# Kernel tuning notes

Measured on AMD Instinct MI355X. Metric: run time of the kernel, lower is better.

The kernel has to match this reference:

```python
import jax, jax.numpy as jnp
import numpy as np

DIM = 64
NB = 32
LEFT, RIGHT = -1.0, 1.0
EPS_BIN = 0.01
EPS_SLOPE = 0.01


def setup_inputs() -> dict:
    key = jax.random.key(0)
    ks = jax.random.split(key, 10)
    m, cdim, hid = 16384, 64, 100
    x = jax.random.uniform(ks[0], (m, DIM), minval=LEFT + 1e-3, maxval=RIGHT - 1e-3)
    cond = jax.random.normal(ks[1], (m, cdim))
    def dense(k, i, o, scale=1.0):
        return (jax.random.normal(k, (i, o)) * (scale / np.sqrt(i))).astype(jnp.float32)
    inp = dict(
        x=x, cond=cond,
        periodic_mask=jnp.ones((1, DIM), dtype=jnp.int32),
        w_W1=dense(ks[2], cdim, hid), w_b1=jnp.zeros((hid,), jnp.float32),
        w_W2=dense(ks[3], hid, DIM * NB, 0.1), w_b2=jnp.zeros((DIM * NB,), jnp.float32),
        h_W1=dense(ks[4], cdim, hid), h_b1=jnp.zeros((hid,), jnp.float32),
        h_W2=dense(ks[5], hid, DIM * NB, 0.1), h_b2=jnp.zeros((DIM * NB,), jnp.float32),
        s_W1=dense(ks[6], cdim, hid), s_b1=jnp.zeros((hid,), jnp.float32),
        s_W2=dense(ks[7], hid, DIM * (NB + 1), 0.1), s_b2=jnp.zeros((DIM * (NB + 1),), jnp.float32),
    )
    return inp


def _mlp(c, W1, b1, W2, b2):
    return jax.nn.silu(c @ W1 + b1) @ W2 + b2


def _rq_spline(x, w_logit, h_logit, d_raw, periodic_mask):
    # x: [m, dim]; w/h: [m, dim, NB]; d: [m, dim, NB+1]
    widths = EPS_BIN + (1.0 - EPS_BIN * NB) * jax.nn.softmax(w_logit, axis=-1)
    heights = EPS_BIN + (1.0 - EPS_BIN * NB) * jax.nn.softmax(h_logit, axis=-1)
    derivs = EPS_SLOPE + jax.nn.softplus(d_raw)  # [m, dim, NB+1]
    # periodic dims: tie boundary slopes (last == first)
    pm = periodic_mask.astype(bool)  # [1, dim]
    derivs = derivs.at[..., -1].set(jnp.where(pm, derivs[..., 0], derivs[..., -1]))

    span = RIGHT - LEFT
    cw = LEFT + span * jnp.concatenate(
        [jnp.zeros_like(widths[..., :1]), jnp.cumsum(widths, axis=-1)], axis=-1)
    ch = LEFT + span * jnp.concatenate(
        [jnp.zeros_like(heights[..., :1]), jnp.cumsum(heights, axis=-1)], axis=-1)
    cw = cw.at[..., 0].set(LEFT).at[..., -1].set(RIGHT)
    ch = ch.at[..., 0].set(LEFT).at[..., -1].set(RIGHT)
    wk_all = cw[..., 1:] - cw[..., :-1]   # actual bin widths
    hk_all = ch[..., 1:] - ch[..., :-1]   # actual bin heights

    # bin search: number of interior knots <= x
    idx = jnp.sum((x[..., None] >= cw[..., 1:-1]).astype(jnp.int32), axis=-1)
    idx = jnp.clip(idx, 0, NB - 1)[..., None]  # [m, dim, 1]

    gather = lambda a: jnp.take_along_axis(a, idx, axis=-1)[..., 0]
    cwk = gather(cw[..., :-1])
    chk = gather(ch[..., :-1])
    wk = gather(wk_all)
    hk = gather(hk_all)
    dk = gather(derivs[..., :-1])
    dk1 = gather(derivs[..., 1:])

    delta = hk / wk
    theta = (x - cwk) / wk
    t1m = theta * (1.0 - theta)
    denom = delta + (dk1 + dk - 2.0 * delta) * t1m
    y = chk + hk * (delta * theta * theta + dk * t1m) / denom
    deriv = (delta * delta) * (dk1 * theta * theta + 2.0 * delta * t1m
                               + dk * (1.0 - theta) * (1.0 - theta)) / (denom * denom)
    ladJ = jnp.sum(jnp.log(deriv), axis=-1, keepdims=True)  # [m, 1]
    return y, ladJ


def reference(x, cond, periodic_mask, w_W1, w_b1, w_W2, w_b2,
              h_W1, h_b1, h_W2, h_b2, s_W1, s_b1, s_W2, s_b2):
    m = x.shape[0]
    w = _mlp(cond, w_W1, w_b1, w_W2, w_b2).reshape(m, DIM, NB)
    h = _mlp(cond, h_W1, h_b1, h_W2, h_b2).reshape(m, DIM, NB)
    s = _mlp(cond, s_W1, s_b1, s_W2, s_b2).reshape(m, DIM, NB + 1)
    return _rq_spline(x, w, h, s, periodic_mask)
```

## Files before the change

### kernel.cpp

```cpp
#include <hip/hip_runtime.h>
#include <stdint.h>

#define M_TOTAL 16384
#define DIMS    64
#define CDIM    64
#define HID     100
#define ROWS    32
#define LOG2E   1.4426950408889634f
#define LN2     0.6931471805599453f

typedef __bf16 bf16x8 __attribute__((ext_vector_type(8)));
typedef float  f32x4  __attribute__((ext_vector_type(4)));

#define BKG        14
#define CN_STRIDE  (BKG*16*8)
#define DIM_STRIDE (7*CN_STRIDE)
#define W2M_ELEMS  (DIMS*DIM_STRIDE)
#define B2ALL_ELEMS (DIMS*128)
#define W1M_ELEMS  (3*7*8*16*8)
#define B1_ELEMS   (3*112)
#define W2M_OFF   0
#define B2ALL_OFF (W2M_ELEMS*2)
#define W1M_OFF   (B2ALL_OFF + B2ALL_ELEMS*4)
#define B1_OFF    (W1M_OFF + W1M_ELEMS*2)

__device__ __forceinline__ uint16_t f2bf(float f) {
  uint32_t u = __float_as_uint(f);
  return (uint16_t)((u + 0x8000u) >> 16);
}

__global__ void repack_kernel(
    const float* __restrict__ wW2, const float* __restrict__ wb2,
    const float* __restrict__ hW2, const float* __restrict__ hb2,
    const float* __restrict__ sW2, const float* __restrict__ sb2,
    const float* __restrict__ wW1, const float* __restrict__ hW1,
    const float* __restrict__ sW1,
    const float* __restrict__ wb1, const float* __restrict__ hb1,
    const float* __restrict__ sb1,
    uint16_t* __restrict__ W2m, float* __restrict__ b2all,
    uint16_t* __restrict__ W1m, float* __restrict__ b1all)
{
  int i = blockIdx.x * 256 + threadIdx.x;
  if (i < W2M_ELEMS) {
    int j  = i & 7;
    int c  = (i >> 3) & 15;
    int t  = i >> 7;
    int kg = t % BKG;
    int t2 = t / BKG;
    int cn = t2 % 7;
    int d  = t2 / 7;
    int k   = kg*8 + j;
    int col = cn*16 + c;
    float v = 0.f;
    if (k < HID) {
      if (col < 32)      v = wW2[k*2048 + d*32 + col] * LOG2E;
      else if (col < 64) v = hW2[k*2048 + d*32 + (col-32)] * LOG2E;
      else if (col < 97) v = sW2[k*2112 + d*33 + (col-64)];
    }
    W2m[i] = f2bf(v);
    return;
  }
  i -= W2M_ELEMS;
  if (i < B2ALL_ELEMS) {
    int c = i & 127;
    int d = i >> 7;
    float v = 0.f;
    if (c < 32)      v = wb2[d*32 + c] * LOG2E;
    else if (c < 64) v = hb2[d*32 + (c-32)] * LOG2E;
    else if (c < 97) v = sb2[d*33 + (c-64)];
    b2all[i] = v;
    return;
  }
  i -= B2ALL_ELEMS;
  if (i < W1M_ELEMS) {
    int jj = i & 7;
    int c  = (i >> 3) & 15;
    int kg = (i >> 7) & 7;
    int t  = i >> 10;
    int cn = t % 7;
    int mat = t / 7;
    int j = cn*16 + c;
    int k = kg*8 + jj;
    const float* W1 = (mat == 0) ? wW1 : (mat == 1) ? hW1 : sW1;
    W1m[i] = f2bf((j < HID) ? W1[k*HID + j] : 0.f);
    return;
  }
  i -= W1M_ELEMS;
  if (i < B1_ELEMS) {
    int mat = i / 112, col = i % 112;
    const float* b1 = (mat == 0) ? wb1 : (mat == 1) ? hb1 : sb1;
    b1all[i] = (col < HID) ? b1[col] : 0.f;
  }
}

__global__ __launch_bounds__(256, 2)
void spline_main(
    const float* __restrict__ X, const float* __restrict__ C,
    const int* __restrict__ pmask,
    const uint16_t* __restrict__ W2m, const float* __restrict__ b2all,
    const uint16_t* __restrict__ W1m, const float* __restrict__ b1all,
    float* __restrict__ Y, float* __restrict__ LADJ)
{
  __shared__ union {
    float cond_s[ROWS*68];
    float Ls[4][ROWS*100];
  } U;
  __shared__ uint16_t At[3*16*ROWS*8];
  __shared__ float LjLds[4][ROWS];

  const int tid = threadIdx.x;
  const int r0 = blockIdx.x * ROWS;
  const int lane = tid & 63, wv = tid >> 6;
  const int l15 = lane & 15, lkg = lane >> 4;
  const int hb = lane >> 5;
  const int srow = lane & 31;

  for (int i = tid; i < ROWS*CDIM; i += 256) {
    int r = i >> 6, c = i & 63;
    U.cond_s[r*68 + c] = C[(size_t)(r0 + r)*CDIM + c];
  }
  __syncthreads();

  {
    bf16x8 cf[2][2];
#pragma unroll
    for (int m = 0; m < 2; ++m)
#pragma unroll
      for (int ks = 0; ks < 2; ++ks) {
        const float* cp = &U.cond_s[(m*16 + l15)*68 + ks*32 + lkg*8];
        float4 c0 = *(const float4*)cp;
        float4 c1 = *(const float4*)(cp + 4);
        union { uint16_t u[8]; bf16x8 v; } tmp;
        tmp.u[0]=f2bf(c0.x); tmp.u[1]=f2bf(c0.y); tmp.u[2]=f2bf(c0.z); tmp.u[3]=f2bf(c0.w);
        tmp.u[4]=f2bf(c1.x); tmp.u[5]=f2bf(c1.y); tmp.u[6]=f2bf(c1.z); tmp.u[7]=f2bf(c1.w);
        cf[m][ks] = tmp.v;
      }
    for (int t = wv; t < 21; t += 4) {
      int mat = t / 7, cn = t % 7;
      const uint16_t* Wb = W1m + (size_t)(mat*7 + cn)*1024;
      bf16x8 wf[2];
#pragma unroll
      for (int ks = 0; ks < 2; ++ks)
        wf[ks] = *(const bf16x8*)&Wb[(ks*4 + lkg)*128 + l15*8];
      f32x4 h0 = {0.f,0.f,0.f,0.f}, h1 = {0.f,0.f,0.f,0.f};
#pragma unroll
      for (int ks = 0; ks < 2; ++ks) {
        h0 = __builtin_amdgcn_mfma_f32_16x16x32_bf16(cf[0][ks], wf[ks], h0, 0, 0, 0);
        h1 = __builtin_amdgcn_mfma_f32_16x16x32_bf16(cf[1][ks], wf[ks], h1, 0, 0, 0);
      }
      float bb = b1all[mat*112 + cn*16 + l15];
      int j = cn*16 + l15;
      int base = mat*4096 + (j >> 3)*256 + (j & 7);
#pragma unroll
      for (int r = 0; r < 4; ++r) {
        float a0 = h0[r] + bb;
        float v0 = a0 * __builtin_amdgcn_rcpf(1.f + __builtin_amdgcn_exp2f(-LOG2E*a0));
        At[base + (lkg*4 + r)*8] = f2bf(v0);
        float a1 = h1[r] + bb;
        float v1 = a1 * __builtin_amdgcn_rcpf(1.f + __builtin_amdgcn_exp2f(-LOG2E*a1));
        At[base + (16 + lkg*4 + r)*8] = f2bf(v1);
      }
    }
    for (int i2 = tid; i2 < 768; i2 += 256) {
      int mat = i2 >> 8, q = i2 & 255;
      *(uint32_t*)&At[mat*4096 + 14*256 + q*2] = 0u;
    }
  }
  __syncthreads();

  float* LsW = &U.Ls[wv][0];
  const int dbase = wv*16;
  float ladj2 = 0.f;
  float xq = 0.f; int pq = 0;

  auto SPLINE = [&](int d, float xv, int pm) {
    const float* Lr = LsW + srow*100 + hb*32;
    float e[32];
#pragma unroll
    for (int q = 0; q < 8; ++q) *(float4*)&e[4*q] = *(const float4*)(Lr + 4*q);
    float t2[16], t4[8], t8[4], t16[2];
#pragma unroll
    for (int k = 0; k < 16; ++k) t2[k] = e[2*k] + e[2*k+1];
#pragma unroll
    for (int k = 0; k < 8; ++k)  t4[k] = t2[2*k] + t2[2*k+1];
#pragma unroll
    for (int k = 0; k < 4; ++k)  t8[k] = t4[2*k] + t4[2*k+1];
    t16[0] = t8[0] + t8[1]; t16[1] = t8[2] + t8[3];
    float S = t16[0] + t16[1];
    float rs = __builtin_amdgcn_rcpf(S);
    float Aa = (xv + 1.f) * 0.7352941176470588f * S;
    float Uq = 0.014705882352941176f * S;

    float T = Aa, p = 0.f, fidx;
    {
      float A = fmaf(-16.f, Uq, T);
      bool c4 = t16[0] <= A;
      p = c4 ? t16[0] : p;  T = c4 ? A : T;

      float n8 = c4 ? t8[2] : t8[0];
      A = fmaf(-8.f, Uq, T);
      float tt = p + n8;
      bool c3 = tt <= A;
      p = c3 ? tt : p;  T = c3 ? A : T;

      float n4 = c4 ? (c3 ? t4[6] : t4[4]) : (c3 ? t4[2] : t4[0]);
      A = fmaf(-4.f, Uq, T);
      tt = p + n4;
      bool c2 = tt <= A;
      p = c2 ? tt : p;  T = c2 ? A : T;

      float n2 = c4 ? (c3 ? (c2 ? t2[14] : t2[12]) : (c2 ? t2[10] : t2[8]))
                    : (c3 ? (c2 ? t2[6]  : t2[4])  : (c2 ? t2[2]  : t2[0]));
      A = fmaf(-2.f, Uq, T);
      tt = p + n2;
      bool c1 = tt <= A;
      p = c1 ? tt : p;  T = c1 ? A : T;

      float n1 = c4 ? (c3 ? (c2 ? (c1 ? e[30] : e[28]) : (c1 ? e[26] : e[24]))
                          : (c2 ? (c1 ? e[22] : e[20]) : (c1 ? e[18] : e[16])))
                    : (c3 ? (c2 ? (c1 ? e[14] : e[12]) : (c1 ? e[10] : e[8]))
                          : (c2 ? (c1 ? e[6]  : e[4])  : (c1 ? e[2]  : e[0])));
      A = fmaf(-1.f, Uq, T);
      bool c0 = (p + n1) <= A;
      fidx = (c4 ? 16.f : 0.f) + (c3 ? 8.f : 0.f) + (c2 ? 4.f : 0.f)
           + (c1 ? 2.f : 0.f) + (c0 ? 1.f : 0.f);
    }
    float idxu = __shfl(fidx, srow);
    bool B4 = idxu >= 15.5f; float u = B4 ? idxu - 16.f : idxu;
    bool B3 = u >= 7.5f;  u = B3 ? u - 8.f : u;
    bool B2 = u >= 3.5f;  u = B2 ? u - 4.f : u;
    bool B1 = u >= 1.5f;  u = B1 ? u - 2.f : u;
    bool B0 = u >= 0.5f;
    float Psel = B4 ? t16[0] : 0.f;
    float q8 = B4 ? t8[2] : t8[0];
    Psel = B3 ? Psel + q8 : Psel;
    float q4 = B4 ? (B3 ? t4[6] : t4[4]) : (B3 ? t4[2] : t4[0]);
    Psel = B2 ? Psel + q4 : Psel;
    float q2 = B4 ? (B3 ? (B2 ? t2[14] : t2[12]) : (B2 ? t2[10] : t2[8]))
                  : (B3 ? (B2 ? t2[6]  : t2[4])  : (B2 ? t2[2]  : t2[0]));
    Psel = B1 ? Psel + q2 : Psel;
    float q1e = B4 ? (B3 ? (B2 ? (B1 ? e[28] : e[24]) : (B1 ? e[20] : e[16]))
                         : (B2 ? (B1 ? e[12] : e[8])  : (B1 ? e[4]  : e[0])))
                   : (B3 ? (B2 ? (B1 ? e[28-16] : e[24-16]) : (B1 ? e[4] : e[0])) : 0.f);
    q1e = B4 ? (B3 ? (B2 ? (B1 ? e[30-2] : e[26-2]) : (B1 ? e[22-2] : e[18-2]))
                   : (B2 ? (B1 ? e[14+16-2] : e[10+16-2]) : (B1 ? e[6+16-2] : e[2+16-2])))
             : (B3 ? (B2 ? (B1 ? e[14] : e[12]) : (B1 ? e[10] : e[8]))
                   : (B2 ? (B1 ? e[6] : e[4]) : (B1 ? e[2] : e[0])));
    {
      float a0_ = B1 ? e[2]  : e[0];
      float a1_ = B1 ? e[6]  : e[4];
      float a2_ = B1 ? e[10] : e[8];
      float a3_ = B1 ? e[14] : e[12];
      float a4_ = B1 ? e[18] : e[16];
      float a5_ = B1 ? e[22] : e[20];
      float a6_ = B1 ? e[26] : e[24];
      float a7_ = B1 ? e[30] : e[28];
      float b0_ = B2 ? a1_ : a0_;
      float b1_ = B2 ? a3_ : a2_;
      float b2_ = B2 ? a5_ : a4_;
      float b3_ = B2 ? a7_ : a6_;
      float c0_ = B3 ? b1_ : b0_;
      float c1_ = B3 ? b3_ : b2_;
      q1e = B4 ? c1_ : c0_;
    }
    float q1o;
    {
      float a0_ = B1 ? e[3]  : e[1];
      float a1_ = B1 ? e[7]  : e[5];
      float a2_ = B1 ? e[11] : e[9];
      float a3_ = B1 ? e[15] : e[13];
      float a4_ = B1 ? e[19] : e[17];
      float a5_ = B1 ? e[23] : e[21];
      float a6_ = B1 ? e[27] : e[25];
      float a7_ = B1 ? e[31] : e[29];
      float b0_ = B2 ? a1_ : a0_;
      float b1_ = B2 ? a3_ : a2_;
      float b2_ = B2 ? a5_ : a4_;
      float b3_ = B2 ? a7_ : a6_;
      float c0_ = B3 ? b1_ : b0_;
      float c1_ = B3 ? b3_ : b2_;
      q1o = B4 ? c1_ : c0_;
    }
    Psel = B0 ? Psel + q1e : Psel;
    float esel = B0 ? q1o : q1e;

    float cK = fmaf(0.02f, idxu, -1.f) + 1.36f*rs*Psel;
    float wK = (idxu > 30.5f) ? (1.f - cK) : fmaf(1.36f*rs, esel, 0.02f);
    int idxi = (int)idxu;
    int off = 64 + idxi + hb;
    if (hb && idxi == 31) off = pm ? 64 : 96;
    float sl = LsW[srow*100 + off];
    float dkv = fmaf(LN2, __builtin_amdgcn_logf(1.f + __builtin_amdgcn_exp2f(LOG2E*sl)), 0.01f);
    float cO = __shfl_xor(cK, 32);
    float wO = __shfl_xor(wK, 32);
    float dO = __shfl_xor(dkv, 32);
    float cwk = cK, wk = wK, dk = dkv, chk = cO, hk = wO, dk1 = dO;
    float rw = __builtin_amdgcn_rcpf(wk);
    float th = (xv - cwk)*rw;
    float delta = hk*rw;
    float omt = 1.f - th, t1m = th*omt, th2 = th*th;
    float denom = fmaf(dk1 + dk - 2.f*delta, t1m, delta);
    float rden = __builtin_amdgcn_rcpf(denom);
    float yv = fmaf(hk*fmaf(delta, th2, dk*t1m), rden, chk);
    float dn2 = fmaf(dk1, th2, fmaf(2.f*delta, t1m, dk*omt*omt));
    ladj2 += 2.f*(__builtin_amdgcn_logf(delta) - __builtin_amdgcn_logf(denom))
           + __builtin_amdgcn_logf(dn2);
    if (!hb) Y[(size_t)(r0 + srow)*DIMS + d] = yv;
  };

  auto LOADA = [&](bf16x8 (&a2)[2][4], int mat) {
#pragma unroll
    for (int m = 0; m < 2; ++m)
#pragma unroll
      for (int ks = 0; ks < 4; ++ks)
        a2[m][ks] = *(const bf16x8*)&At[mat*4096 + (ks*4 + lkg)*256 + (m*16 + l15)*8];
  };

  auto DO = [&](const bf16x8 (&afm)[2][4], const bf16x8 (&B)[4],
                float bb, int col, bool doexp) {
    f32x4 a0 = {bb,bb,bb,bb}, a1 = {bb,bb,bb,bb};
#pragma unroll
    for (int ks = 0; ks < 4; ++ks)
      a0 = __builtin_amdgcn_mfma_f32_16x16x32_bf16(afm[0][ks], B[ks], a0, 0, 0, 0);
#pragma unroll
    for (int ks = 0; ks < 4; ++ks)
      a1 = __builtin_amdgcn_mfma_f32_16x16x32_bf16(afm[1][ks], B[ks], a1, 0, 0, 0);
    if (doexp) {
#pragma unroll
      for (int r = 0; r < 4; ++r) {
        a0[r] = __builtin_amdgcn_exp2f(a0[r]);
        a1[r] = __builtin_amdgcn_exp2f(a1[r]);
      }
    }
    if (col < 97) {
#pragma unroll
      for (int r = 0; r < 4; ++r) {
        LsW[(lkg*4 + r)*100 + col]      = a0[r];
        LsW[(16 + lkg*4 + r)*100 + col] = a1[r];
      }
    }
  };

#pragma unroll 1
  for (int dd = 0; dd < 16; ++dd) {
    const int d = dbase + dd;
    const uint16_t* Bd = W2m + (size_t)d*DIM_STRIDE;
    auto LOADB = [&](bf16x8 (&dst)[4], int cn) {
#pragma unroll
      for (int ks = 0; ks < 4; ++ks) {
        int kgb = ks*4 + lkg; kgb = (kgb > 13) ? 13 : kgb;
        dst[ks] = *(const bf16x8*)&Bd[cn*CN_STRIDE + kgb*128 + l15*8];
      }
    };
    bf16x8 bA[4], bB[4], bC[4];
    LOADB(bA, 0); LOADB(bB, 1); LOADB(bC, 2);
    float bbv[7];
#pragma unroll
    for (int cn = 0; cn < 7; ++cn) bbv[cn] = b2all[d*128 + cn*16 + l15];
    float xn = X[(size_t)(r0 + srow)*DIMS + d];
    int pn = pmask[d];

    if (dd > 0) SPLINE(d - 1, xq, pq);
    xq = xn; pq = pn;

    bf16x8 afc[2][4];
    LOADA(afc, 0);
    DO(afc, bA, bbv[0], 0*16 + l15, true);  LOADB(bA, 3);
    DO(afc, bB, bbv[1], 1*16 + l15, true);  LOADB(bB, 4);
    LOADA(afc, 1);
    DO(afc, bC, bbv[2], 2*16 + l15, true);  LOADB(bC, 5);
    DO(afc, bA, bbv[3], 3*16 + l15, true);  LOADB(bA, 6);
    LOADA(afc, 2);
    DO(afc, bB, bbv[4], 4*16 + l15, false);
    DO(afc, bC, bbv[5], 5*16 + l15, false);
    DO(afc, bA, bbv[6], 6*16 + l15, false);
  }
  SPLINE(dbase + 15, xq, pq);

  if (!hb) LjLds[wv][srow] = ladj2;
  __syncthreads();
  if (tid < ROWS)
    LADJ[r0 + tid] = LN2 * ((LjLds[0][tid] + LjLds[1][tid]) + (LjLds[2][tid] + LjLds[3][tid]));
}

extern "C" void kernel_launch(void* const* d_in, const int* in_sizes, int n_in,
                              void* d_out, int out_size, void* d_ws, size_t ws_size,
                              hipStream_t stream) {
  const float* x     = (const float*)d_in[0];
  const float* cond  = (const float*)d_in[1];
  const int*   pmask = (const int*)d_in[2];
  const float* wW1 = (const float*)d_in[3];
  const float* wb1 = (const float*)d_in[4];
  const float* wW2 = (const float*)d_in[5];
  const float* wb2 = (const float*)d_in[6];
  const float* hW1 = (const float*)d_in[7];
  const float* hb1 = (const float*)d_in[8];
  const float* hW2 = (const float*)d_in[9];
  const float* hb2 = (const float*)d_in[10];
  const float* sW1 = (const float*)d_in[11];
  const float* sb1 = (const float*)d_in[12];
  const float* sW2 = (const float*)d_in[13];
  const float* sb2 = (const float*)d_in[14];

  uint16_t* W2m   = (uint16_t*)((char*)d_ws + W2M_OFF);
  float*    b2all = (float*)((char*)d_ws + B2ALL_OFF);
  uint16_t* W1m   = (uint16_t*)((char*)d_ws + W1M_OFF);
  float*    b1all = (float*)((char*)d_ws + B1_OFF);

  const int total = W2M_ELEMS + B2ALL_ELEMS + W1M_ELEMS + B1_ELEMS;
  repack_kernel<<<(total + 255)/256, 256, 0, stream>>>(
      wW2, wb2, hW2, hb2, sW2, sb2, wW1, hW1, sW1, wb1, hb1, sb1,
      W2m, b2all, W1m, b1all);

  float* Y = (float*)d_out;
  float* LADJ = Y + (size_t)M_TOTAL*DIMS;
  spline_main<<<M_TOTAL/ROWS, 256, 0, stream>>>(
      x, cond, pmask, W2m, b2all, W1m, b1all, Y, LADJ);
}
```

Measured before the change: 60.05 us.

## Shrink LDS with fp16 logit staging and trimmed activation tile for occupancy

The per-wave logit scratch buffer now holds half-precision values instead of floats. The hidden-activation tile drops its zero-padded k-groups, going from 16 to 13 groups, and the A-fragment load reuses group 12 for the last k-step, relying on the padded W2 rows being zero. Together these roughly halve shared-memory use per block, which lets launch bounds ask for three blocks per CU instead of two, improving latency hiding. The cost is fp16 rounding of exponentiated logits and slope values, and a tighter register budget that could cause spills.

```diff
diff --git a/kernel.cpp b/kernel.cpp
--- a/kernel.cpp
+++ b/kernel.cpp
@@ -1,4 +1,5 @@
 #include <hip/hip_runtime.h>
+#include <hip/hip_fp16.h>
 #include <stdint.h>
 
 #define M_TOTAL 16384
@@ -93,7 +94,7 @@
   }
 }
 
-__global__ __launch_bounds__(256, 2)
+__global__ __launch_bounds__(256, 3)
 void spline_main(
     const float* __restrict__ X, const float* __restrict__ C,
     const int* __restrict__ pmask,
@@ -103,9 +104,9 @@
 {
   __shared__ union {
     float cond_s[ROWS*68];
-    float Ls[4][ROWS*100];
+    __half Ls[4][ROWS*100];
   } U;
-  __shared__ uint16_t At[3*16*ROWS*8];
+  __shared__ uint16_t At[3*13*ROWS*8];
   __shared__ float LjLds[4][ROWS];
 
   const int tid = threadIdx.x;
@@ -150,34 +151,36 @@
       }
       float bb = b1all[mat*112 + cn*16 + l15];
       int j = cn*16 + l15;
-      int base = mat*4096 + (j >> 3)*256 + (j & 7);
-#pragma unroll
-      for (int r = 0; r < 4; ++r) {
-        float a0 = h0[r] + bb;
-        float v0 = a0 * __builtin_amdgcn_rcpf(1.f + __builtin_amdgcn_exp2f(-LOG2E*a0));
-        At[base + (lkg*4 + r)*8] = f2bf(v0);
-        float a1 = h1[r] + bb;
-        float v1 = a1 * __builtin_amdgcn_rcpf(1.f + __builtin_amdgcn_exp2f(-LOG2E*a1));
-        At[base + (16 + lkg*4 + r)*8] = f2bf(v1);
-      }
-    }
-    for (int i2 = tid; i2 < 768; i2 += 256) {
-      int mat = i2 >> 8, q = i2 & 255;
-      *(uint32_t*)&At[mat*4096 + 14*256 + q*2] = 0u;
+      if ((j >> 3) <= 12) {
+        int base = mat*3328 + (j >> 3)*256 + (j & 7);
+#pragma unroll
+        for (int r = 0; r < 4; ++r) {
+          float a0 = h0[r] + bb;
+          float v0 = a0 * __builtin_amdgcn_rcpf(1.f + __builtin_amdgcn_exp2f(-LOG2E*a0));
+          At[base + (lkg*4 + r)*8] = f2bf(v0);
+          float a1 = h1[r] + bb;
+          float v1 = a1 * __builtin_amdgcn_rcpf(1.f + __builtin_amdgcn_exp2f(-LOG2E*a1));
+          At[base + (16 + lkg*4 + r)*8] = f2bf(v1);
+        }
+      }
     }
   }
   __syncthreads();
 
-  float* LsW = &U.Ls[wv][0];
+  __half* LsW = &U.Ls[wv][0];
   const int dbase = wv*16;
   float ladj2 = 0.f;
   float xq = 0.f; int pq = 0;
 
   auto SPLINE = [&](int d, float xv, int pm) {
-    const float* Lr = LsW + srow*100 + hb*32;
+    const __half* Lr = LsW + srow*100 + hb*32;
     float e[32];
 #pragma unroll
-    for (int q = 0; q < 8; ++q) *(float4*)&e[4*q] = *(const float4*)(Lr + 4*q);
+    for (int q = 0; q < 16; ++q) {
+      __half2 hp = *(const __half2*)(Lr + 2*q);
+      float2 f2 = __half22float2(hp);
+      e[2*q] = f2.x; e[2*q+1] = f2.y;
+    }
     float t2[16], t4[8], t8[4], t16[2];
 #pragma unroll
     for (int k = 0; k < 16; ++k) t2[k] = e[2*k] + e[2*k+1];
@@ -239,13 +242,7 @@
     float q2 = B4 ? (B3 ? (B2 ? t2[14] : t2[12]) : (B2 ? t2[10] : t2[8]))
                   : (B3 ? (B2 ? t2[6]  : t2[4])  : (B2 ? t2[2]  : t2[0]));
     Psel = B1 ? Psel + q2 : Psel;
-    float q1e = B4 ? (B3 ? (B2 ? (B1 ? e[28] : e[24]) : (B1 ? e[20] : e[16]))
-                         : (B2 ? (B1 ? e[12] : e[8])  : (B1 ? e[4]  : e[0])))
-                   : (B3 ? (B2 ? (B1 ? e[28-16] : e[24-16]) : (B1 ? e[4] : e[0])) : 0.f);
-    q1e = B4 ? (B3 ? (B2 ? (B1 ? e[30-2] : e[26-2]) : (B1 ? e[22-2] : e[18-2]))
-                   : (B2 ? (B1 ? e[14+16-2] : e[10+16-2]) : (B1 ? e[6+16-2] : e[2+16-2])))
-             : (B3 ? (B2 ? (B1 ? e[14] : e[12]) : (B1 ? e[10] : e[8]))
-                   : (B2 ? (B1 ? e[6] : e[4]) : (B1 ? e[2] : e[0])));
+    float q1e, q1o;
     {
       float a0_ = B1 ? e[2]  : e[0];
       float a1_ = B1 ? e[6]  : e[4];
@@ -263,7 +260,6 @@
       float c1_ = B3 ? b3_ : b2_;
       q1e = B4 ? c1_ : c0_;
     }
-    float q1o;
     {
       float a0_ = B1 ? e[3]  : e[1];
       float a1_ = B1 ? e[7]  : e[5];
@@ -289,7 +285,7 @@
     int idxi = (int)idxu;
     int off = 64 + idxi + hb;
     if (hb && idxi == 31) off = pm ? 64 : 96;
-    float sl = LsW[srow*100 + off];
+    float sl = __half2float(LsW[srow*100 + off]);
     float dkv = fmaf(LN2, __builtin_amdgcn_logf(1.f + __builtin_amdgcn_exp2f(LOG2E*sl)), 0.01f);
     float cO = __shfl_xor(cK, 32);
     float wO = __shfl_xor(wK, 32);
@@ -309,11 +305,14 @@
   };
 
   auto LOADA = [&](bf16x8 (&a2)[2][4], int mat) {
-#pragma unroll
-    for (int m = 0; m < 2; ++m)
-#pragma unroll
-      for (int ks = 0; ks < 4; ++ks)
-        a2[m][ks] = *(const bf16x8*)&At[mat*4096 + (ks*4 + lkg)*256 + (m*16 + l15)*8];
+    const uint16_t* base = &At[mat*3328];
+#pragma unroll
+    for (int m = 0; m < 2; ++m) {
+#pragma unroll
+      for (int ks = 0; ks < 3; ++ks)
+        a2[m][ks] = *(const bf16x8*)&base[(ks*4 + lkg)*256 + (m*16 + l15)*8];
+      a2[m][3] = *(const bf16x8*)&base[12*256 + (m*16 + l15)*8];
+    }
   };
 
   auto DO = [&](const bf16x8 (&afm)[2][4], const bf16x8 (&B)[4],
@@ -335,8 +334,8 @@
     if (col < 97) {
 #pragma unroll
       for (int r = 0; r < 4; ++r) {
-        LsW[(lkg*4 + r)*100 + col]      = a0[r];
-        LsW[(16 + lkg*4 + r)*100 + col] = a1[r];
+        LsW[(lkg*4 + r)*100 + col]      = __float2half(a0[r]);
+        LsW[(16 + lkg*4 + r)*100 + col] = __float2half(a1[r]);
       }
     }
   };
```

New measurement: 65.42 us. 8.9% more time.

## Software-pipeline W2 fragment loads across dims with a four-buffer rotation

Applied to the files above, without the earlier changes.

The per-dimension loop now keeps four B-fragment register buffers and rotates them, prefetching the first four column blocks of the next dimension while the current dimension's last blocks compute. The loop is unrolled by four so buffer roles rotate statically. This hides the global-load latency at the start of each dimension, at the cost of more live VGPRs (one extra buffer), which could lower occupancy. Dead code computing an unused q1e expression is also removed.

```diff
diff --git a/kernel.cpp b/kernel.cpp
--- a/kernel.cpp
+++ b/kernel.cpp
@@ -239,13 +239,7 @@
     float q2 = B4 ? (B3 ? (B2 ? t2[14] : t2[12]) : (B2 ? t2[10] : t2[8]))
                   : (B3 ? (B2 ? t2[6]  : t2[4])  : (B2 ? t2[2]  : t2[0]));
     Psel = B1 ? Psel + q2 : Psel;
-    float q1e = B4 ? (B3 ? (B2 ? (B1 ? e[28] : e[24]) : (B1 ? e[20] : e[16]))
-                         : (B2 ? (B1 ? e[12] : e[8])  : (B1 ? e[4]  : e[0])))
-                   : (B3 ? (B2 ? (B1 ? e[28-16] : e[24-16]) : (B1 ? e[4] : e[0])) : 0.f);
-    q1e = B4 ? (B3 ? (B2 ? (B1 ? e[30-2] : e[26-2]) : (B1 ? e[22-2] : e[18-2]))
-                   : (B2 ? (B1 ? e[14+16-2] : e[10+16-2]) : (B1 ? e[6+16-2] : e[2+16-2])))
-             : (B3 ? (B2 ? (B1 ? e[14] : e[12]) : (B1 ? e[10] : e[8]))
-                   : (B2 ? (B1 ? e[6] : e[4]) : (B1 ? e[2] : e[0])));
+    float q1e, q1o;
     {
       float a0_ = B1 ? e[2]  : e[0];
       float a1_ = B1 ? e[6]  : e[4];
@@ -263,7 +257,6 @@
       float c1_ = B3 ? b3_ : b2_;
       q1e = B4 ? c1_ : c0_;
     }
-    float q1o;
     {
       float a0_ = B1 ? e[3]  : e[1];
       float a1_ = B1 ? e[7]  : e[5];
@@ -341,39 +334,49 @@
     }
   };
 
-#pragma unroll 1
-  for (int dd = 0; dd < 16; ++dd) {
-    const int d = dbase + dd;
+  auto LOADB = [&](bf16x8 (&dst)[4], int d, int cn) {
     const uint16_t* Bd = W2m + (size_t)d*DIM_STRIDE;
-    auto LOADB = [&](bf16x8 (&dst)[4], int cn) {
-#pragma unroll
-      for (int ks = 0; ks < 4; ++ks) {
-        int kgb = ks*4 + lkg; kgb = (kgb > 13) ? 13 : kgb;
-        dst[ks] = *(const bf16x8*)&Bd[cn*CN_STRIDE + kgb*128 + l15*8];
-      }
-    };
-    bf16x8 bA[4], bB[4], bC[4];
-    LOADB(bA, 0); LOADB(bB, 1); LOADB(bC, 2);
+#pragma unroll
+    for (int ks = 0; ks < 4; ++ks) {
+      int kgb = ks*4 + lkg; kgb = (kgb > 13) ? 13 : kgb;
+      dst[ks] = *(const bf16x8*)&Bd[cn*CN_STRIDE + kgb*128 + l15*8];
+    }
+  };
+
+  auto DIM = [&](int d, bf16x8 (&u0)[4], bf16x8 (&u1)[4],
+                 bf16x8 (&u2)[4], bf16x8 (&u3)[4]) {
     float bbv[7];
 #pragma unroll
     for (int cn = 0; cn < 7; ++cn) bbv[cn] = b2all[d*128 + cn*16 + l15];
     float xn = X[(size_t)(r0 + srow)*DIMS + d];
     int pn = pmask[d];
 
-    if (dd > 0) SPLINE(d - 1, xq, pq);
+    if (d > dbase) SPLINE(d - 1, xq, pq);
     xq = xn; pq = pn;
 
+    const int dnx = (d + 1) & 63;
     bf16x8 afc[2][4];
     LOADA(afc, 0);
-    DO(afc, bA, bbv[0], 0*16 + l15, true);  LOADB(bA, 3);
-    DO(afc, bB, bbv[1], 1*16 + l15, true);  LOADB(bB, 4);
+    DO(afc, u0, bbv[0], 0*16 + l15, true);  LOADB(u0, d,   4);
+    DO(afc, u1, bbv[1], 1*16 + l15, true);  LOADB(u1, d,   5);
     LOADA(afc, 1);
-    DO(afc, bC, bbv[2], 2*16 + l15, true);  LOADB(bC, 5);
-    DO(afc, bA, bbv[3], 3*16 + l15, true);  LOADB(bA, 6);
+    DO(afc, u2, bbv[2], 2*16 + l15, true);  LOADB(u2, d,   6);
+    DO(afc, u3, bbv[3], 3*16 + l15, true);  LOADB(u3, dnx, 0);
     LOADA(afc, 2);
-    DO(afc, bB, bbv[4], 4*16 + l15, false);
-    DO(afc, bC, bbv[5], 5*16 + l15, false);
-    DO(afc, bA, bbv[6], 6*16 + l15, false);
+    DO(afc, u0, bbv[4], 4*16 + l15, false); LOADB(u0, dnx, 1);
+    DO(afc, u1, bbv[5], 5*16 + l15, false); LOADB(u1, dnx, 2);
+    DO(afc, u2, bbv[6], 6*16 + l15, false); LOADB(u2, dnx, 3);
+  };
+
+  bf16x8 b0[4], b1[4], b2[4], b3[4];
+  LOADB(b0, dbase, 0); LOADB(b1, dbase, 1); LOADB(b2, dbase, 2); LOADB(b3, dbase, 3);
+#pragma unroll 1
+  for (int dg = 0; dg < 4; ++dg) {
+    const int d0 = dbase + dg*4;
+    DIM(d0 + 0, b0, b1, b2, b3);
+    DIM(d0 + 1, b3, b0, b1, b2);
+    DIM(d0 + 2, b2, b3, b0, b1);
+    DIM(d0 + 3, b1, b2, b3, b0);
   }
   SPLINE(dbase + 15, xq, pq);
 
```

New measurement: 75.16 us. 1.25x slower.
